# Kernel optimization log

Hardware: AMD Instinct MI355X
Metric: run time of the kernel (lower is better)

The kernel has to match this reference:

```python
import jax, jax.numpy as jnp
import numpy as np

B, I, H = 64, 512, 1024


def _linear_params(k, out_dim, in_dim):
    kw, kb = jax.random.split(k)
    bound = 1.0 / np.sqrt(in_dim)
    W = jax.random.uniform(kw, (out_dim, in_dim), minval=-bound, maxval=bound)
    b = jax.random.uniform(kb, (out_dim,), minval=-bound, maxval=bound)
    return W, b


def setup_inputs() -> dict:
    key = jax.random.key(0)
    ks = jax.random.split(key, 14)
    items = jax.random.normal(ks[0], (B, I), dtype=jnp.float32)
    plastic_weights = 0.01 * jax.random.normal(ks[1], (B, H, H), dtype=jnp.float32)
    reward = jax.random.normal(ks[2], (B, 1), dtype=jnp.float32)
    We, be = _linear_params(ks[3], H, I)          # embedding_layer
    W1, b1 = _linear_params(ks[4], H, H)          # extra hidden layer 0
    W2, b2 = _linear_params(ks[5], H, H)          # extra hidden layer 1
    Wfc2, bfc2 = _linear_params(ks[6], H, H)      # fc2
    Whr, bhr = _linear_params(ks[7], H, H)        # hidden_reward_combination_layer
    Wch, bch = _linear_params(ks[8], 1, H)        # choice
    Wr, br = _linear_params(ks[9], H, 1)          # reward_linear
    Wnm, bnm = _linear_params(ks[10], 2, H)       # neuromodulator_out
    Wv, bv = _linear_params(ks[11], 1, H)         # value_out
    alpha = 0.01 * (2.0 * jax.random.uniform(ks[12], (H, H)) - 1.0)
    return dict(items=items, plastic_weights=plastic_weights, reward=reward,
                We=We, be=be, W1=W1, b1=b1, W2=W2, b2=b2,
                Wfc2=Wfc2, bfc2=bfc2, Whr=Whr, bhr=bhr,
                Wch=Wch, bch=bch, Wr=Wr, br=br,
                Wnm=Wnm, bnm=bnm, alpha=alpha, Wv=Wv, bv=bv)


def reference(items, plastic_weights, reward,
              We, be, W1, b1, W2, b2, Wfc2, bfc2, Whr, bhr,
              Wch, bch, Wr, br, Wnm, bnm, alpha, Wv, bv):
    # stacked Linear + tanh
    x = jnp.tanh(items @ We.T + be)            # (B, H)
    x = jnp.tanh(x @ W1.T + b1)
    x = jnp.tanh(x @ W2.T + b2)
    innate = x @ Wfc2.T + bfc2                 # (B, H)
    # plastic contribution: batched matvec with elementwise-scaled weights
    plastic = jnp.einsum('bhi,bi->bh', alpha * plastic_weights, x)
    pre_tanh_hidden = innate + plastic
    hidden = jnp.tanh(pre_tanh_hidden)
    reward_embedding = reward @ Wr.T + br      # (B, H)
    hrc = jnp.tanh((hidden + reward_embedding) @ Whr.T + bhr)
    nm_out = jnp.tanh(hrc @ Wnm.T + bnm)       # (B, 2)
    neuromodulator = (nm_out[:, 0] - nm_out[:, 1])[:, None, None]  # (B,1,1)
    choice = jax.nn.sigmoid(hidden @ Wch.T + bch)  # (B, 1)
    value = hidden @ Wv.T + bv                     # (B, 1)
    hebbian_trace = jnp.tanh(jnp.einsum('bh,bi->bhi', pre_tanh_hidden, x))
    new_pw = jnp.clip(plastic_weights + neuromodulator * hebbian_trace, -50.0, 50.0)
    return (choice, neuromodulator, value, new_pw, hidden)
```

## Files before the change

kernel.cpp:

```cpp
#include <hip/hip_runtime.h>

#define HD 1024
#define BB 64
#define II 512

typedef float f4 __attribute__((ext_vector_type(4)));

__device__ __forceinline__ float fast_tanh(float x) {
    float ax = __builtin_fabsf(x);
    float e  = __builtin_amdgcn_exp2f(ax * -2.8853900817779268f);
    float t  = (1.0f - e) * __builtin_amdgcn_rcpf(1.0f + e);
    return x < 0.0f ? -t : t;
}

template <int K, bool RW>
__global__ __launch_bounds__(1024) void k_gemm(const float* __restrict__ A,
                                               const float* __restrict__ W,
                                               const float* __restrict__ bias,
                                               float* __restrict__ out,
                                               const float* __restrict__ rew,
                                               const float* __restrict__ Wr,
                                               const float* __restrict__ br)
{
    constexpr int J   = K / 256;
    constexpr int LSZ = RW ? 10 * K : 8 * K;
    __shared__ float wlds[LSZ];

    int tid  = threadIdx.x;
    int oct  = blockIdx.x & 127;
    int bg   = blockIdx.x >> 7;
    int h0   = oct * 8;

    {
        const f4* src = (const f4*)(W + (size_t)h0 * K);
        f4* dst = (f4*)wlds;
#pragma unroll
        for (int v = tid; v < 2 * K; v += 1024) dst[v] = src[v];
        if (RW) {
            const f4* wrs = (const f4*)Wr;
            const f4* brs = (const f4*)br;
            f4* d2 = (f4*)(wlds + 8 * K);
            for (int v = tid; v < K / 4; v += 1024) d2[v] = wrs[v];
            f4* d3 = (f4*)(wlds + 9 * K);
            for (int v = tid; v < K / 4; v += 1024) d3[v] = brs[v];
        }
    }
    __syncthreads();

    int lane = tid & 63;
    int wave = tid >> 6;
    int b    = bg * 16 + wave;

    f4 a[J];
    float rb = RW ? rew[b] : 0.0f;
#pragma unroll
    for (int j = 0; j < J; ++j) {
        a[j] = *(const f4*)(A + (size_t)b * K + j * 256 + lane * 4);
        if (RW) {
            f4 wr4 = *(const f4*)(wlds + 8 * K + j * 256 + lane * 4);
            f4 br4 = *(const f4*)(wlds + 9 * K + j * 256 + lane * 4);
            a[j].x += rb * wr4.x + br4.x;
            a[j].y += rb * wr4.y + br4.y;
            a[j].z += rb * wr4.z + br4.z;
            a[j].w += rb * wr4.w + br4.w;
        }
    }
    float acc[8];
#pragma unroll
    for (int hh = 0; hh < 8; ++hh) {
        const float* wrow = wlds + hh * K;
        float s = 0.f;
#pragma unroll
        for (int j = 0; j < J; ++j) {
            f4 w4 = *(const f4*)(wrow + j * 256 + lane * 4);
            s += a[j].x * w4.x + a[j].y * w4.y + a[j].z * w4.z + a[j].w * w4.w;
        }
        acc[hh] = s;
    }
#pragma unroll
    for (int hh = 0; hh < 8; ++hh)
#pragma unroll
        for (int off = 32; off; off >>= 1)
            acc[hh] += __shfl_xor(acc[hh], off, 64);
    if (lane == 0) {
        f4 o0, o1;
        o0.x = fast_tanh(acc[0] + bias[h0 + 0]);
        o0.y = fast_tanh(acc[1] + bias[h0 + 1]);
        o0.z = fast_tanh(acc[2] + bias[h0 + 2]);
        o0.w = fast_tanh(acc[3] + bias[h0 + 3]);
        o1.x = fast_tanh(acc[4] + bias[h0 + 4]);
        o1.y = fast_tanh(acc[5] + bias[h0 + 5]);
        o1.z = fast_tanh(acc[6] + bias[h0 + 6]);
        o1.w = fast_tanh(acc[7] + bias[h0 + 7]);
        *(f4*)(out + (size_t)b * HD + h0)     = o0;
        *(f4*)(out + (size_t)b * HD + h0 + 4) = o1;
    }
}

__global__ __launch_bounds__(512) void k_plastic(const float* __restrict__ pw,
                                                 const float* __restrict__ alpha,
                                                 const float* __restrict__ Wfc2,
                                                 const float* __restrict__ bfc2,
                                                 const float* __restrict__ x,
                                                 float* __restrict__ pre,
                                                 float* __restrict__ hidden)
{
    __shared__ float xs[8][HD];
    int tid  = threadIdx.x;
    int lane = tid & 63;
    int wave = tid >> 6;
    int bg   = blockIdx.x >> 7;
    int hg   = blockIdx.x & 127;
    int b0   = bg * 8;
    int h    = hg * 8 + wave;

#pragma unroll
    for (int v = tid; v < 2048; v += 512) {
        int r = v >> 8, c = (v & 255) * 4;
        *(f4*)&xs[r][c] = *(const f4*)(x + ((b0 + r) << 10) + c);
    }
    __syncthreads();

    const float* ar = alpha + ((size_t)h << 10);
    const float* wr = Wfc2 + ((size_t)h << 10);
    f4 av[4], wv[4];
#pragma unroll
    for (int j = 0; j < 4; ++j) {
        av[j] = *(const f4*)(ar + j * 256 + lane * 4);
        wv[j] = *(const f4*)(wr + j * 256 + lane * 4);
    }
    float bfc = bfc2[h];

#pragma unroll
    for (int bb = 0; bb < 8; ++bb) {
        const float* prow = pw + ((size_t)(b0 + bb) << 20) + ((size_t)h << 10);
        float accp = 0.f, acci = 0.f;
#pragma unroll
        for (int j = 0; j < 4; ++j) {
            f4 p4 = *(const f4*)(prow + j * 256 + lane * 4);
            f4 x4 = *(const f4*)&xs[bb][j * 256 + lane * 4];
            accp += av[j].x * p4.x * x4.x + av[j].y * p4.y * x4.y +
                    av[j].z * p4.z * x4.z + av[j].w * p4.w * x4.w;
            acci += wv[j].x * x4.x + wv[j].y * x4.y + wv[j].z * x4.z + wv[j].w * x4.w;
        }
#pragma unroll
        for (int off = 32; off; off >>= 1) {
            accp += __shfl_xor(accp, off, 64);
            acci += __shfl_xor(acci, off, 64);
        }
        if (lane == 0) {
            float pv = acci + bfc + accp;
            pre[((b0 + bb) << 10) + h]    = pv;
            hidden[((b0 + bb) << 10) + h] = fast_tanh(pv);
        }
    }
}

__global__ __launch_bounds__(256) void k_heads(const float* __restrict__ hidden,
                                               const float* __restrict__ hrc,
                                               const float* __restrict__ Wnm, const float* __restrict__ bnm,
                                               const float* __restrict__ Wch, const float* __restrict__ bch,
                                               const float* __restrict__ Wv,  const float* __restrict__ bv,
                                               float* __restrict__ out_choice,
                                               float* __restrict__ out_nm,
                                               float* __restrict__ out_value,
                                               float* __restrict__ nm_ws) {
    int b = blockIdx.x;
    int tid = threadIdx.x;
    float a0 = 0.f, a1 = 0.f, a2 = 0.f, a3 = 0.f;
    for (int k = tid; k < HD; k += 256) {
        float hv = hidden[(b << 10) + k];
        float rv = hrc[(b << 10) + k];
        a0 += Wnm[k] * rv;
        a1 += Wnm[HD + k] * rv;
        a2 += Wch[k] * hv;
        a3 += Wv[k] * hv;
    }
    int lane = tid & 63, wave = tid >> 6;
#pragma unroll
    for (int off = 32; off; off >>= 1) {
        a0 += __shfl_xor(a0, off, 64);
        a1 += __shfl_xor(a1, off, 64);
        a2 += __shfl_xor(a2, off, 64);
        a3 += __shfl_xor(a3, off, 64);
    }
    __shared__ float red[4][4];
    if (lane == 0) { red[wave][0] = a0; red[wave][1] = a1; red[wave][2] = a2; red[wave][3] = a3; }
    __syncthreads();
    if (tid == 0) {
        float s0 = red[0][0] + red[1][0] + red[2][0] + red[3][0];
        float s1 = red[0][1] + red[1][1] + red[2][1] + red[3][1];
        float s2 = red[0][2] + red[1][2] + red[2][2] + red[3][2];
        float s3 = red[0][3] + red[1][3] + red[2][3] + red[3][3];
        float n0 = fast_tanh(s0 + bnm[0]);
        float n1 = fast_tanh(s1 + bnm[1]);
        float nv = n0 - n1;
        out_nm[b] = nv;
        nm_ws[b]  = nv;
        float z = s2 + bch[0];
        out_choice[b] = __builtin_amdgcn_rcpf(1.0f + __builtin_amdgcn_exp2f(-z * 1.4426950408889634f));
        out_value[b] = s3 + bv[0];
    }
}

__global__ __launch_bounds__(256) void k_update(const float* __restrict__ pw,
                                                const float* __restrict__ pre,
                                                const float* __restrict__ x,
                                                const float* __restrict__ nm,
                                                float* __restrict__ out) {
    const int stride = 8192 * 256;
    int blk = 8191 - (int)blockIdx.x;
#pragma unroll
    for (int it = 7; it >= 0; --it) {
        int f = blk * 256 + threadIdx.x + it * stride;
        size_t e = (size_t)f << 2;
        int b = f >> 18;
        int h = (f >> 8) & 1023;
        int i = (f & 255) << 2;
        f4 p4 = *(const f4*)(pw + e);
        f4 x4 = *(const f4*)(x + (b << 10) + i);
        float ps = pre[(b << 10) + h];
        float nb = nm[b];
        f4 o4;
        o4.x = fminf(fmaxf(p4.x + nb * fast_tanh(ps * x4.x), -50.f), 50.f);
        o4.y = fminf(fmaxf(p4.y + nb * fast_tanh(ps * x4.y), -50.f), 50.f);
        o4.z = fminf(fmaxf(p4.z + nb * fast_tanh(ps * x4.z), -50.f), 50.f);
        o4.w = fminf(fmaxf(p4.w + nb * fast_tanh(ps * x4.w), -50.f), 50.f);
        __builtin_nontemporal_store(o4, (f4*)(out + e));
    }
}

extern "C" void kernel_launch(void* const* d_in, const int* in_sizes, int n_in,
                              void* d_out, int out_size, void* d_ws, size_t ws_size,
                              hipStream_t stream) {
    const float* items  = (const float*)d_in[0];
    const float* pw     = (const float*)d_in[1];
    const float* reward = (const float*)d_in[2];
    const float* We     = (const float*)d_in[3];
    const float* be     = (const float*)d_in[4];
    const float* W1     = (const float*)d_in[5];
    const float* b1     = (const float*)d_in[6];
    const float* W2     = (const float*)d_in[7];
    const float* b2     = (const float*)d_in[8];
    const float* Wfc2   = (const float*)d_in[9];
    const float* bfc2   = (const float*)d_in[10];
    const float* Whr    = (const float*)d_in[11];
    const float* bhr    = (const float*)d_in[12];
    const float* Wch    = (const float*)d_in[13];
    const float* bch    = (const float*)d_in[14];
    const float* Wr     = (const float*)d_in[15];
    const float* br     = (const float*)d_in[16];
    const float* Wnm    = (const float*)d_in[17];
    const float* bnm    = (const float*)d_in[18];
    const float* alpha  = (const float*)d_in[19];
    const float* Wv     = (const float*)d_in[20];
    const float* bv     = (const float*)d_in[21];

    float* ws   = (float*)d_ws;
    float* x0   = ws;
    float* x1   = ws + 65536;
    float* x2   = ws + 131072;
    float* preb = ws + 196608;
    float* hrc  = ws + 262144;
    float* nm   = ws + 327680;

    float* out        = (float*)d_out;
    float* out_choice = out;
    float* out_nm     = out + 64;
    float* out_value  = out + 128;
    float* out_newpw  = out + 192;
    float* out_hidden = out + 192 + BB * HD * HD;

    k_gemm<II, false><<<512, 1024, 0, stream>>>(items, We, be, x0, nullptr, nullptr, nullptr);
    k_gemm<HD, false><<<512, 1024, 0, stream>>>(x0, W1, b1, x1, nullptr, nullptr, nullptr);
    k_gemm<HD, false><<<512, 1024, 0, stream>>>(x1, W2, b2, x2, nullptr, nullptr, nullptr);
    k_plastic<<<1024, 512, 0, stream>>>(pw, alpha, Wfc2, bfc2, x2, preb, out_hidden);
    k_gemm<HD, true><<<512, 1024, 0, stream>>>(out_hidden, Whr, bhr, hrc, reward, Wr, br);
    k_heads<<<64, 256, 0, stream>>>(out_hidden, hrc, Wnm, bnm, Wch, bch, Wv, bv,
                                    out_choice, out_nm, out_value, nm);
    k_update<<<8192, 256, 0, stream>>>(pw, preb, x2, nm, out_newpw);
}
```

Measured before the change: 179.1 us.

## Fuse plastic, hrc, heads and weight update into one persistent kernel with spin sync

Replaces the plastic, hrc GEMM, heads and update kernels with one kernel of 256 blocks, four per batch row. The blocks of a row synchronise through global atomic counters and spin-waits. Each block's slice of the plastic_weights rows is read twice within the same kernel, so the second read may hit cache, and three kernel launches plus the pre/hrc round trips through global memory go away. In exchange, the spin-waits require all four blocks of a row to be co-resident, Whr is now re-read per batch without LDS reuse, and parallelism for the large update pass drops to 256 blocks.

```diff
diff --git a/kernel.cpp b/kernel.cpp
--- a/kernel.cpp
+++ b/kernel.cpp
@@ -13,18 +13,14 @@
     return x < 0.0f ? -t : t;
 }
 
-template <int K, bool RW>
+template <int K>
 __global__ __launch_bounds__(1024) void k_gemm(const float* __restrict__ A,
                                                const float* __restrict__ W,
                                                const float* __restrict__ bias,
-                                               float* __restrict__ out,
-                                               const float* __restrict__ rew,
-                                               const float* __restrict__ Wr,
-                                               const float* __restrict__ br)
+                                               float* __restrict__ out)
 {
-    constexpr int J   = K / 256;
-    constexpr int LSZ = RW ? 10 * K : 8 * K;
-    __shared__ float wlds[LSZ];
+    constexpr int J = K / 256;
+    __shared__ float wlds[8 * K];
 
     int tid  = threadIdx.x;
     int oct  = blockIdx.x & 127;
@@ -36,14 +32,6 @@
         f4* dst = (f4*)wlds;
 #pragma unroll
         for (int v = tid; v < 2 * K; v += 1024) dst[v] = src[v];
-        if (RW) {
-            const f4* wrs = (const f4*)Wr;
-            const f4* brs = (const f4*)br;
-            f4* d2 = (f4*)(wlds + 8 * K);
-            for (int v = tid; v < K / 4; v += 1024) d2[v] = wrs[v];
-            f4* d3 = (f4*)(wlds + 9 * K);
-            for (int v = tid; v < K / 4; v += 1024) d3[v] = brs[v];
-        }
     }
     __syncthreads();
 
@@ -52,19 +40,10 @@
     int b    = bg * 16 + wave;
 
     f4 a[J];
-    float rb = RW ? rew[b] : 0.0f;
-#pragma unroll
-    for (int j = 0; j < J; ++j) {
+#pragma unroll
+    for (int j = 0; j < J; ++j)
         a[j] = *(const f4*)(A + (size_t)b * K + j * 256 + lane * 4);
-        if (RW) {
-            f4 wr4 = *(const f4*)(wlds + 8 * K + j * 256 + lane * 4);
-            f4 br4 = *(const f4*)(wlds + 9 * K + j * 256 + lane * 4);
-            a[j].x += rb * wr4.x + br4.x;
-            a[j].y += rb * wr4.y + br4.y;
-            a[j].z += rb * wr4.z + br4.z;
-            a[j].w += rb * wr4.w + br4.w;
-        }
-    }
+
     float acc[8];
 #pragma unroll
     for (int hh = 0; hh < 8; ++hh) {
@@ -97,51 +76,71 @@
     }
 }
 
-__global__ __launch_bounds__(512) void k_plastic(const float* __restrict__ pw,
-                                                 const float* __restrict__ alpha,
-                                                 const float* __restrict__ Wfc2,
-                                                 const float* __restrict__ bfc2,
-                                                 const float* __restrict__ x,
-                                                 float* __restrict__ pre,
-                                                 float* __restrict__ hidden)
+__global__ __launch_bounds__(256) void k_zero(int* __restrict__ p) {
+    p[threadIdx.x] = 0;
+}
+
+__global__ __launch_bounds__(1024) void k_fused(
+        const float* __restrict__ pw,
+        const float* __restrict__ alpha,
+        const float* __restrict__ Wfc2,
+        const float* __restrict__ bfc2,
+        const float* __restrict__ x2,
+        const float* __restrict__ reward,
+        const float* __restrict__ Wr,
+        const float* __restrict__ br,
+        const float* __restrict__ Whr,
+        const float* __restrict__ bhr,
+        const float* __restrict__ Wnm,
+        const float* __restrict__ bnm,
+        const float* __restrict__ Wch,
+        const float* __restrict__ bch,
+        const float* __restrict__ Wv,
+        const float* __restrict__ bv,
+        float* __restrict__ out_choice,
+        float* __restrict__ out_nm,
+        float* __restrict__ out_value,
+        float* __restrict__ out_newpw,
+        float* __restrict__ out_hidden,
+        float* __restrict__ parts,
+        int*   __restrict__ cnt_p,
+        int*   __restrict__ cnt_h,
+        int*   __restrict__ flag_nm)
 {
-    __shared__ float xs[8][HD];
-    int tid  = threadIdx.x;
-    int lane = tid & 63;
-    int wave = tid >> 6;
-    int bg   = blockIdx.x >> 7;
-    int hg   = blockIdx.x & 127;
-    int b0   = bg * 8;
-    int h    = hg * 8 + wave;
-
-#pragma unroll
-    for (int v = tid; v < 2048; v += 512) {
-        int r = v >> 8, c = (v & 255) * 4;
-        *(f4*)&xs[r][c] = *(const f4*)(x + ((b0 + r) << 10) + c);
-    }
-    __syncthreads();
-
-    const float* ar = alpha + ((size_t)h << 10);
-    const float* wr = Wfc2 + ((size_t)h << 10);
-    f4 av[4], wv[4];
-#pragma unroll
-    for (int j = 0; j < 4; ++j) {
-        av[j] = *(const f4*)(ar + j * 256 + lane * 4);
-        wv[j] = *(const f4*)(wr + j * 256 + lane * 4);
-    }
-    float bfc = bfc2[h];
-
-#pragma unroll
-    for (int bb = 0; bb < 8; ++bb) {
-        const float* prow = pw + ((size_t)(b0 + bb) << 20) + ((size_t)h << 10);
+    __shared__ float xs[HD];
+    __shared__ float pre_s[256];
+    __shared__ float hid_s[256];
+    __shared__ float hplus[HD];
+    __shared__ float wred[16][4];
+    __shared__ float nm_lds;
+
+    int tid   = threadIdx.x;
+    int lane  = tid & 63;
+    int wave  = tid >> 6;
+    int b     = blockIdx.x >> 2;
+    int sub   = blockIdx.x & 3;
+    int hbase = sub << 8;
+
+    if (tid < 256) ((f4*)xs)[tid] = ((const f4*)(x2 + ((size_t)b << 10)))[tid];
+    __syncthreads();
+
+    for (int rr = 0; rr < 16; ++rr) {
+        int hl = (wave << 4) + rr;
+        int h  = hbase + hl;
+        const float* prow = pw + ((size_t)b << 20) + ((size_t)h << 10);
+        const float* ar   = alpha + ((size_t)h << 10);
+        const float* wr   = Wfc2 + ((size_t)h << 10);
         float accp = 0.f, acci = 0.f;
 #pragma unroll
         for (int j = 0; j < 4; ++j) {
-            f4 p4 = *(const f4*)(prow + j * 256 + lane * 4);
-            f4 x4 = *(const f4*)&xs[bb][j * 256 + lane * 4];
-            accp += av[j].x * p4.x * x4.x + av[j].y * p4.y * x4.y +
-                    av[j].z * p4.z * x4.z + av[j].w * p4.w * x4.w;
-            acci += wv[j].x * x4.x + wv[j].y * x4.y + wv[j].z * x4.z + wv[j].w * x4.w;
+            int i = j * 256 + lane * 4;
+            f4 p4 = *(const f4*)(prow + i);
+            f4 a4 = *(const f4*)(ar + i);
+            f4 w4 = *(const f4*)(wr + i);
+            f4 x4 = *(const f4*)(xs + i);
+            accp += a4.x * p4.x * x4.x + a4.y * p4.y * x4.y +
+                    a4.z * p4.z * x4.z + a4.w * p4.w * x4.w;
+            acci += w4.x * x4.x + w4.y * x4.y + w4.z * x4.z + w4.w * x4.w;
         }
 #pragma unroll
         for (int off = 32; off; off >>= 1) {
@@ -149,84 +148,114 @@
             acci += __shfl_xor(acci, off, 64);
         }
         if (lane == 0) {
-            float pv = acci + bfc + accp;
-            pre[((b0 + bb) << 10) + h]    = pv;
-            hidden[((b0 + bb) << 10) + h] = fast_tanh(pv);
-        }
-    }
-}
-
-__global__ __launch_bounds__(256) void k_heads(const float* __restrict__ hidden,
-                                               const float* __restrict__ hrc,
-                                               const float* __restrict__ Wnm, const float* __restrict__ bnm,
-                                               const float* __restrict__ Wch, const float* __restrict__ bch,
-                                               const float* __restrict__ Wv,  const float* __restrict__ bv,
-                                               float* __restrict__ out_choice,
-                                               float* __restrict__ out_nm,
-                                               float* __restrict__ out_value,
-                                               float* __restrict__ nm_ws) {
-    int b = blockIdx.x;
-    int tid = threadIdx.x;
-    float a0 = 0.f, a1 = 0.f, a2 = 0.f, a3 = 0.f;
-    for (int k = tid; k < HD; k += 256) {
-        float hv = hidden[(b << 10) + k];
-        float rv = hrc[(b << 10) + k];
-        a0 += Wnm[k] * rv;
-        a1 += Wnm[HD + k] * rv;
-        a2 += Wch[k] * hv;
-        a3 += Wv[k] * hv;
-    }
-    int lane = tid & 63, wave = tid >> 6;
+            float pv = acci + bfc2[h] + accp;
+            float hv = fast_tanh(pv);
+            pre_s[hl] = pv;
+            hid_s[hl] = hv;
+            out_hidden[(b << 10) + h] = hv;
+        }
+    }
+    __syncthreads();
+    if (tid == 0) {
+        __threadfence();
+        __hip_atomic_fetch_add(&cnt_p[b], 1, __ATOMIC_ACQ_REL, __HIP_MEMORY_SCOPE_AGENT);
+        while (__hip_atomic_load(&cnt_p[b], __ATOMIC_ACQUIRE, __HIP_MEMORY_SCOPE_AGENT) < 4)
+            __builtin_amdgcn_s_sleep(1);
+    }
+    __syncthreads();
+
+    float rwd = reward[b];
+    hplus[tid] = out_hidden[(b << 10) + tid] + rwd * Wr[tid] + br[tid];
+    __syncthreads();
+
+    float nm0 = 0.f, nm1 = 0.f;
+    for (int rr = 0; rr < 16; ++rr) {
+        int h2 = hbase + (wave << 4) + rr;
+        const float* wrow = Whr + ((size_t)h2 << 10);
+        float s = 0.f;
+#pragma unroll
+        for (int j = 0; j < 4; ++j) {
+            int i = j * 256 + lane * 4;
+            f4 w4 = *(const f4*)(wrow + i);
+            f4 h4 = *(const f4*)(hplus + i);
+            s += w4.x * h4.x + w4.y * h4.y + w4.z * h4.z + w4.w * h4.w;
+        }
+#pragma unroll
+        for (int off = 32; off; off >>= 1) s += __shfl_xor(s, off, 64);
+        float hrcv = fast_tanh(s + bhr[h2]);
+        if (lane == 0) {
+            nm0 += Wnm[h2] * hrcv;
+            nm1 += Wnm[HD + h2] * hrcv;
+        }
+    }
+    float cv = 0.f, vv = 0.f;
+    if (tid < 256) {
+        cv = Wch[hbase + tid] * hid_s[tid];
+        vv = Wv[hbase + tid] * hid_s[tid];
+    }
 #pragma unroll
     for (int off = 32; off; off >>= 1) {
-        a0 += __shfl_xor(a0, off, 64);
-        a1 += __shfl_xor(a1, off, 64);
-        a2 += __shfl_xor(a2, off, 64);
-        a3 += __shfl_xor(a3, off, 64);
-    }
-    __shared__ float red[4][4];
-    if (lane == 0) { red[wave][0] = a0; red[wave][1] = a1; red[wave][2] = a2; red[wave][3] = a3; }
+        cv += __shfl_xor(cv, off, 64);
+        vv += __shfl_xor(vv, off, 64);
+    }
+    if (lane == 0) {
+        wred[wave][0] = nm0; wred[wave][1] = nm1;
+        wred[wave][2] = cv;  wred[wave][3] = vv;
+    }
     __syncthreads();
     if (tid == 0) {
-        float s0 = red[0][0] + red[1][0] + red[2][0] + red[3][0];
-        float s1 = red[0][1] + red[1][1] + red[2][1] + red[3][1];
-        float s2 = red[0][2] + red[1][2] + red[2][2] + red[3][2];
-        float s3 = red[0][3] + red[1][3] + red[2][3] + red[3][3];
-        float n0 = fast_tanh(s0 + bnm[0]);
-        float n1 = fast_tanh(s1 + bnm[1]);
-        float nv = n0 - n1;
-        out_nm[b] = nv;
-        nm_ws[b]  = nv;
-        float z = s2 + bch[0];
-        out_choice[b] = __builtin_amdgcn_rcpf(1.0f + __builtin_amdgcn_exp2f(-z * 1.4426950408889634f));
-        out_value[b] = s3 + bv[0];
-    }
-}
-
-__global__ __launch_bounds__(256) void k_update(const float* __restrict__ pw,
-                                                const float* __restrict__ pre,
-                                                const float* __restrict__ x,
-                                                const float* __restrict__ nm,
-                                                float* __restrict__ out) {
-    const int stride = 8192 * 256;
-    int blk = 8191 - (int)blockIdx.x;
-#pragma unroll
-    for (int it = 7; it >= 0; --it) {
-        int f = blk * 256 + threadIdx.x + it * stride;
-        size_t e = (size_t)f << 2;
-        int b = f >> 18;
-        int h = (f >> 8) & 1023;
-        int i = (f & 255) << 2;
-        f4 p4 = *(const f4*)(pw + e);
-        f4 x4 = *(const f4*)(x + (b << 10) + i);
-        float ps = pre[(b << 10) + h];
-        float nb = nm[b];
-        f4 o4;
-        o4.x = fminf(fmaxf(p4.x + nb * fast_tanh(ps * x4.x), -50.f), 50.f);
-        o4.y = fminf(fmaxf(p4.y + nb * fast_tanh(ps * x4.y), -50.f), 50.f);
-        o4.z = fminf(fmaxf(p4.z + nb * fast_tanh(ps * x4.z), -50.f), 50.f);
-        o4.w = fminf(fmaxf(p4.w + nb * fast_tanh(ps * x4.w), -50.f), 50.f);
-        __builtin_nontemporal_store(o4, (f4*)(out + e));
+        float p0 = 0.f, p1 = 0.f, p2 = 0.f, p3 = 0.f;
+        for (int w = 0; w < 16; ++w) {
+            p0 += wred[w][0]; p1 += wred[w][1];
+            p2 += wred[w][2]; p3 += wred[w][3];
+        }
+        float* pb = parts + b * 16 + sub * 4;
+        pb[0] = p0; pb[1] = p1; pb[2] = p2; pb[3] = p3;
+        __threadfence();
+        __hip_atomic_fetch_add(&cnt_h[b], 1, __ATOMIC_ACQ_REL, __HIP_MEMORY_SCOPE_AGENT);
+        if (sub == 0) {
+            while (__hip_atomic_load(&cnt_h[b], __ATOMIC_ACQUIRE, __HIP_MEMORY_SCOPE_AGENT) < 4)
+                __builtin_amdgcn_s_sleep(1);
+            __threadfence();
+            float s0 = 0.f, s1 = 0.f, s2 = 0.f, s3 = 0.f;
+            for (int q = 0; q < 4; ++q) {
+                const float* pp = parts + b * 16 + q * 4;
+                s0 += pp[0]; s1 += pp[1]; s2 += pp[2]; s3 += pp[3];
+            }
+            float n0 = fast_tanh(s0 + bnm[0]);
+            float n1 = fast_tanh(s1 + bnm[1]);
+            float nv = n0 - n1;
+            out_nm[b] = nv;
+            float z = s2 + bch[0];
+            out_choice[b] = __builtin_amdgcn_rcpf(1.0f + __builtin_amdgcn_exp2f(-z * 1.4426950408889634f));
+            out_value[b]  = s3 + bv[0];
+            __threadfence();
+            __hip_atomic_store(&flag_nm[b], 1, __ATOMIC_RELEASE, __HIP_MEMORY_SCOPE_AGENT);
+        }
+        while (__hip_atomic_load(&flag_nm[b], __ATOMIC_ACQUIRE, __HIP_MEMORY_SCOPE_AGENT) == 0)
+            __builtin_amdgcn_s_sleep(1);
+        nm_lds = out_nm[b];
+    }
+    __syncthreads();
+    float nb = nm_lds;
+
+    for (int rr = 0; rr < 16; ++rr) {
+        int hl = (wave << 4) + rr;
+        int h  = hbase + hl;
+        float ps = pre_s[hl];
+        size_t base = ((size_t)b << 20) + ((size_t)h << 10);
+#pragma unroll
+        for (int j = 0; j < 4; ++j) {
+            int i = j * 256 + lane * 4;
+            f4 p4 = *(const f4*)(pw + base + i);
+            f4 x4 = *(const f4*)(xs + i);
+            f4 o4;
+            o4.x = fminf(fmaxf(p4.x + nb * fast_tanh(ps * x4.x), -50.f), 50.f);
+            o4.y = fminf(fmaxf(p4.y + nb * fast_tanh(ps * x4.y), -50.f), 50.f);
+            o4.z = fminf(fmaxf(p4.z + nb * fast_tanh(ps * x4.z), -50.f), 50.f);
+            o4.w = fminf(fmaxf(p4.w + nb * fast_tanh(ps * x4.w), -50.f), 50.f);
+            __builtin_nontemporal_store(o4, (f4*)(out_newpw + base + i));
+        }
     }
 }
 
@@ -256,13 +285,15 @@
     const float* Wv     = (const float*)d_in[20];
     const float* bv     = (const float*)d_in[21];
 
-    float* ws   = (float*)d_ws;
-    float* x0   = ws;
-    float* x1   = ws + 65536;
-    float* x2   = ws + 131072;
-    float* preb = ws + 196608;
-    float* hrc  = ws + 262144;
-    float* nm   = ws + 327680;
+    float* ws    = (float*)d_ws;
+    float* x0    = ws;
+    float* x1    = ws + 65536;
+    float* x2    = ws + 131072;
+    float* parts = ws + 196608;
+    int*   syncb = (int*)(ws + 197632);
+    int*   cnt_p   = syncb;
+    int*   cnt_h   = syncb + 64;
+    int*   flag_nm = syncb + 128;
 
     float* out        = (float*)d_out;
     float* out_choice = out;
@@ -271,12 +302,12 @@
     float* out_newpw  = out + 192;
     float* out_hidden = out + 192 + BB * HD * HD;
 
-    k_gemm<II, false><<<512, 1024, 0, stream>>>(items, We, be, x0, nullptr, nullptr, nullptr);
-    k_gemm<HD, false><<<512, 1024, 0, stream>>>(x0, W1, b1, x1, nullptr, nullptr, nullptr);
-    k_gemm<HD, false><<<512, 1024, 0, stream>>>(x1, W2, b2, x2, nullptr, nullptr, nullptr);
-    k_plastic<<<1024, 512, 0, stream>>>(pw, alpha, Wfc2, bfc2, x2, preb, out_hidden);
-    k_gemm<HD, true><<<512, 1024, 0, stream>>>(out_hidden, Whr, bhr, hrc, reward, Wr, br);
-    k_heads<<<64, 256, 0, stream>>>(out_hidden, hrc, Wnm, bnm, Wch, bch, Wv, bv,
-                                    out_choice, out_nm, out_value, nm);
-    k_update<<<8192, 256, 0, stream>>>(pw, preb, x2, nm, out_newpw);
-}
+    k_zero<<<1, 256, 0, stream>>>(syncb);
+    k_gemm<II><<<512, 1024, 0, stream>>>(items, We, be, x0);
+    k_gemm<HD><<<512, 1024, 0, stream>>>(x0, W1, b1, x1);
+    k_gemm<HD><<<512, 1024, 0, stream>>>(x1, W2, b2, x2);
+    k_fused<<<256, 1024, 0, stream>>>(pw, alpha, Wfc2, bfc2, x2, reward, Wr, br,
+                                      Whr, bhr, Wnm, bnm, Wch, bch, Wv, bv,
+                                      out_choice, out_nm, out_value, out_newpw,
+                                      out_hidden, parts, cnt_p, cnt_h, flag_nm);
+}
```

Result: slower. 257.6 us (+43.9%).
